# Optimization experiments

Hardware: AMD Instinct MI355X
Metric: run time of the kernel (lower is better)

## Reference

```python
import jax, jax.numpy as jnp
import numpy as np

N_HEADS = 8
D_K = 256
SCALE = D_K ** -0.5


def setup_inputs() -> dict:
    key = jax.random.key(0)
    k1, k2, k3 = jax.random.split(key, 3)
    B, C, H, W = 8, 256, 32, 32
    x = jax.random.normal(k1, (B, C, H, W), dtype=jnp.float32)
    Wp = jax.random.normal(k2, (C, N_HEADS * D_K * 3), dtype=jnp.float32) * (C ** -0.5)
    bp = jnp.zeros((N_HEADS * D_K * 3,), dtype=jnp.float32)
    Wo = jax.random.normal(k3, (N_HEADS * D_K, C), dtype=jnp.float32) * ((N_HEADS * D_K) ** -0.5)
    bo = jnp.zeros((C,), dtype=jnp.float32)
    return {"x": x, "Wp": Wp, "bp": bp, "Wo": Wo, "bo": bo}


def reference(x, Wp, bp, Wo, bo):
    B, C, H, W = x.shape
    S = H * W
    # [B,C,H,W] -> [B,S,C] tokens
    xt = x.reshape(B, C, S).transpose(0, 2, 1)
    qkv = (xt @ Wp + bp).reshape(B, S, N_HEADS, 3 * D_K)
    q, k, v = jnp.split(qkv, 3, axis=-1)  # each [B,S,H,dk]
    attn = jnp.einsum('bihd,bjhd->bijh', q, k) * SCALE
    attn = jax.nn.softmax(attn, axis=2)  # over j (keys)
    res = jnp.einsum('bijh,bjhd->bihd', attn, v).reshape(B, S, N_HEADS * D_K)
    res = res @ Wo + bo + xt  # residual
    return res.transpose(0, 2, 1).reshape(B, C, H, W)
```

## Files before the change

### kernel.cpp

```cpp
#include <hip/hip_runtime.h>

#define NH    8
#define DK    256
#define SS    1024
#define QSCALE 0.09016844136947155f
#define TSH   8192

using frag8  = __attribute__((ext_vector_type(8))) short;
using f32x4  = __attribute__((ext_vector_type(4))) float;
using f32x16 = __attribute__((ext_vector_type(16))) float;

__device__ __forceinline__ unsigned short f2bf(float f) {
    unsigned int u = __float_as_uint(f);
    return (unsigned short)((u + 0x7FFFu + ((u >> 16) & 1u)) >> 16);
}

__device__ __forceinline__ void load_lds16(const void* g, void* l) {
    __builtin_amdgcn_global_load_lds(
        (const __attribute__((address_space(1))) unsigned int*)g,
        (__attribute__((address_space(3))) unsigned int*)l, 16, 0, 0);
}


__global__ __launch_bounds__(256) void k0_t(const float* __restrict__ in,
                                            unsigned short* __restrict__ out,
                                            int R, int C)
{
    __shared__ float tile[32][33];
    const int bz = blockIdx.z;
    const int c0 = blockIdx.x * 32, r0 = blockIdx.y * 32;
    const int tx = threadIdx.x & 31, ty = threadIdx.x >> 5;
    const float* ip = in + (size_t)bz * R * C;
    unsigned short* op = out + (size_t)bz * R * C;
#pragma unroll
    for (int j = 0; j < 4; j++)
        tile[ty + j * 8][tx] = ip[(size_t)(r0 + ty + j * 8) * C + c0 + tx];
    __syncthreads();
#pragma unroll
    for (int j = 0; j < 4; j++)
        op[(size_t)(c0 + ty + j * 8) * R + r0 + tx] = f2bf(tile[tx][ty + j * 8]);
}

__global__ __launch_bounds__(256) void k1_qkv(
    const unsigned short* __restrict__ xb, const unsigned short* __restrict__ Wpt,
    const float* __restrict__ bp,
    unsigned short* __restrict__ qb, unsigned short* __restrict__ kb,
    unsigned short* __restrict__ vb)
{
    __shared__ unsigned short As[128 * 32];
    __shared__ unsigned short Bs[128 * 32];
    const int t = threadIdx.x;
    const int wave = t >> 6, lane = t & 63;
    const int quad = lane >> 4, l16 = lane & 15;
    const int n0 = blockIdx.x * 128, m0 = blockIdx.y * 128;
    const int b = m0 >> 10, s0 = m0 & 1023;
    const int mq = (wave >> 1) * 64, nq = (wave & 1) * 64;
    const int lr = lane >> 2, lc = (lane & 3) * 8;

    const unsigned short* Ag = xb + (size_t)(b * 1024 + s0) * 256;
    const unsigned short* Bg = Wpt + (size_t)n0 * 256;

    f32x4 acc[4][4];
#pragma unroll
    for (int i = 0; i < 4; i++)
#pragma unroll
        for (int j = 0; j < 4; j++) acc[i][j] = (f32x4){0.f, 0.f, 0.f, 0.f};

    for (int k0 = 0; k0 < 256; k0 += 32) {
#pragma unroll
        for (int j = 0; j < 2; j++) {
            int ch = wave + j * 4;
            load_lds16(Ag + (size_t)(ch * 16 + lr) * 256 + k0 + lc, &As[ch * 512]);
            load_lds16(Bg + (size_t)(ch * 16 + lr) * 256 + k0 + lc, &Bs[ch * 512]);
        }
        __syncthreads();
        frag8 af[4], bf[4];
#pragma unroll
        for (int i = 0; i < 4; i++)
            af[i] = *(const frag8*)(&As[(mq + i * 16 + l16) * 32 + quad * 8]);
#pragma unroll
        for (int j = 0; j < 4; j++)
            bf[j] = *(const frag8*)(&Bs[(nq + j * 16 + l16) * 32 + quad * 8]);
#pragma unroll
        for (int i = 0; i < 4; i++)
#pragma unroll
            for (int j = 0; j < 4; j++)
                acc[i][j] = __builtin_amdgcn_mfma_f32_16x16x32_bf16(af[i], bf[j], acc[i][j], 0, 0, 0);
        __syncthreads();
    }

    const int h = n0 / 768;
    const int rem = n0 - h * 768;
    const int tt = rem >> 8;
    const int dbase = (rem & 255) + nq;
    const size_t bh = (size_t)(b * NH + h);
    float bias[4];
#pragma unroll
    for (int j = 0; j < 4; j++) bias[j] = bp[n0 + nq + j * 16 + l16];

    if (tt < 2) {
        const float sc = (tt == 0) ? QSCALE : 1.0f;
        unsigned short* dst = (tt == 0 ? qb : kb) + bh * 32 * TSH;
#pragma unroll
        for (int i = 0; i < 4; i++)
#pragma unroll
            for (int r = 0; r < 4; r++) {
                int s = s0 + mq + i * 16 + quad * 4 + r;
                const size_t tb = (size_t)(s >> 5) * TSH + (s & 31) * 8;
#pragma unroll
                for (int j = 0; j < 4; j++) {
                    int d = dbase + j * 16 + l16;
                    dst[tb + (d >> 3) * 256 + (d & 7)] = f2bf((acc[i][j][r] + bias[j]) * sc);
                }
            }
    } else {
        unsigned short* dst = vb + bh * 32 * TSH;
#pragma unroll
        for (int j = 0; j < 4; j++) {
            int d = dbase + j * 16 + l16;
#pragma unroll
            for (int i = 0; i < 4; i++)
#pragma unroll
                for (int r = 0; r < 4; r++) {
                    int s = s0 + mq + i * 16 + quad * 4 + r;
                    dst[(size_t)(s >> 5) * TSH + ((s >> 3) & 3) * 2048 + d * 8 + (s & 7)]
                        = f2bf(acc[i][j][r] + bias[j]);
                }
        }
    }
}

__global__ __launch_bounds__(256, 2) void k2_attn(
    const unsigned short* __restrict__ qb, const unsigned short* __restrict__ kb,
    const unsigned short* __restrict__ vb, unsigned short* __restrict__ ob)
{
    __shared__ unsigned short Ks[2][TSH];
    __shared__ unsigned short Vs[2][TSH];

    const int t = threadIdx.x;
    const int wave = t >> 6, lane = t & 63;
    const int l32 = lane & 31, hw = lane >> 5;

    const int flat = blockIdx.x;
    const int xcd = flat & 7, tt2 = flat >> 3;
    const int qt = tt2 & 7;
    const int bh = xcd * 8 + (tt2 >> 3);

    const int qrow0 = qt * 128 + wave * 32;

    frag8 qf[16];
    {
        const unsigned short* qp = qb + ((size_t)bh * 32 + qt * 4 + wave) * TSH
                                 + hw * 256 + l32 * 8;
#pragma unroll
        for (int s = 0; s < 16; s++) qf[s] = *(const frag8*)(qp + s * 512);
    }

    f32x16 acc[8];
#pragma unroll
    for (int nb = 0; nb < 8; nb++)
#pragma unroll
        for (int r = 0; r < 16; r++) acc[nb][r] = 0.f;
    float lsum = 0.f;

    const unsigned short* kt0 = kb + (size_t)bh * 32 * TSH;
    const unsigned short* vt0 = vb + (size_t)bh * 32 * TSH;

#pragma unroll
    for (int j = 0; j < 4; j++) {
        int c = wave * 4 + j;
        load_lds16(kt0 + c * 512 + lane * 8, &Ks[0][c * 512]);
        load_lds16(vt0 + c * 512 + lane * 8, &Vs[0][c * 512]);
    }
    __syncthreads();

    for (int kt = 0; kt < 32; kt++) {
        const int cur = kt & 1;

        if (kt < 31) {
            const unsigned short* kg = kt0 + (size_t)(kt + 1) * TSH;
            const unsigned short* vg = vt0 + (size_t)(kt + 1) * TSH;
#pragma unroll
            for (int j = 0; j < 4; j++) {
                int c = wave * 4 + j;
                load_lds16(kg + c * 512 + lane * 8, &Ks[cur ^ 1][c * 512]);
                load_lds16(vg + c * 512 + lane * 8, &Vs[cur ^ 1][c * 512]);
            }
        }

        f32x16 sa0, sa1;
#pragma unroll
        for (int r = 0; r < 16; r++) { sa0[r] = 0.f; sa1[r] = 0.f; }
#pragma unroll
        for (int s = 0; s < 16; s += 2) {
            frag8 kf0 = *(const frag8*)(&Ks[cur][(2 * s + hw) * 256 + l32 * 8]);
            frag8 kf1 = *(const frag8*)(&Ks[cur][(2 * s + 2 + hw) * 256 + l32 * 8]);
            sa0 = __builtin_amdgcn_mfma_f32_32x32x16_bf16(kf0, qf[s], sa0, 0, 0, 0);
            sa1 = __builtin_amdgcn_mfma_f32_32x32x16_bf16(kf1, qf[s + 1], sa1, 0, 0, 0);
        }

        frag8 pf[2];
#pragma unroll
        for (int half = 0; half < 2; half++) {
            float p[8], px[8];
#pragma unroll
            for (int e = 0; e < 8; e++) {
                p[e] = exp2f(sa0[half * 8 + e] + sa1[half * 8 + e]);
                lsum += p[e];
            }
#pragma unroll
            for (int e = 0; e < 8; e++) px[e] = __shfl_xor(p[e], 32);
            frag8 w;
#pragma unroll
            for (int j = 0; j < 4; j++) {
                w[j]     = (short)f2bf(hw ? px[4 + j] : p[j]);
                w[4 + j] = (short)f2bf(hw ? p[4 + j] : px[j]);
            }
            pf[half] = w;
        }

#pragma unroll
        for (int s01 = 0; s01 < 2; s01++)
#pragma unroll
            for (int nb = 0; nb < 8; nb++) {
                frag8 vf = *(const frag8*)(&Vs[cur][(s01 * 2 + hw) * 2048 + (nb * 32 + l32) * 8]);
                acc[nb] = __builtin_amdgcn_mfma_f32_32x32x16_bf16(pf[s01], vf, acc[nb], 0, 0, 0);
            }

        __syncthreads();
    }

    lsum += __shfl_xor(lsum, 32);
    const float linv = 1.f / lsum;

    unsigned short* og = ob + ((size_t)bh * SS + qrow0) * DK + l32;
#pragma unroll
    for (int r = 0; r < 16; r++) {
        const int rowl = (r & 3) + 8 * (r >> 2) + 4 * hw;
        const float li = __shfl(linv, rowl, 64);
        unsigned short* orow = og + (size_t)rowl * DK;
#pragma unroll
        for (int nb = 0; nb < 8; nb++)
            orow[nb * 32] = f2bf(acc[nb][r] * li);
    }
}

__global__ __launch_bounds__(256) void k3_proj(
    const unsigned short* __restrict__ ob, const unsigned short* __restrict__ Wot,
    const float* __restrict__ bo, const float* __restrict__ x,
    float* __restrict__ out)
{
    __shared__ unsigned short As[64 * 32];
    __shared__ unsigned short Bs[64 * 32];
    const int t = threadIdx.x;
    const int wave = t >> 6, lane = t & 63;
    const int quad = lane >> 4, l16 = lane & 15;
    const int n0 = blockIdx.x * 64, m0 = blockIdx.y * 64;
    const int b = m0 >> 10, s0 = m0 & 1023;
    const int mq = (wave >> 1) * 32, nq = (wave & 1) * 32;
    const int lr = lane >> 2, lc = (lane & 3) * 8;

    const unsigned short* Bg = Wot + (size_t)n0 * 2048;

    f32x4 acc[2][2];
#pragma unroll
    for (int i = 0; i < 2; i++)
#pragma unroll
        for (int j = 0; j < 2; j++) acc[i][j] = (f32x4){0.f, 0.f, 0.f, 0.f};

    for (int k0 = 0; k0 < 2048; k0 += 32) {
        const int h = k0 >> 8, d0 = k0 & 255;
        const unsigned short* Ag = ob + (size_t)((b * 8 + h) * 1024 + s0) * 256 + d0;
        load_lds16(Ag + (size_t)(wave * 16 + lr) * 256 + lc, &As[wave * 512]);
        load_lds16(Bg + (size_t)(wave * 16 + lr) * 2048 + k0 + lc, &Bs[wave * 512]);
        __syncthreads();
        frag8 af[2], bf[2];
#pragma unroll
        for (int i = 0; i < 2; i++)
            af[i] = *(const frag8*)(&As[(mq + i * 16 + l16) * 32 + quad * 8]);
#pragma unroll
        for (int j = 0; j < 2; j++)
            bf[j] = *(const frag8*)(&Bs[(nq + j * 16 + l16) * 32 + quad * 8]);
#pragma unroll
        for (int i = 0; i < 2; i++)
#pragma unroll
            for (int j = 0; j < 2; j++)
                acc[i][j] = __builtin_amdgcn_mfma_f32_16x16x32_bf16(af[i], bf[j], acc[i][j], 0, 0, 0);
        __syncthreads();
    }

#pragma unroll
    for (int j = 0; j < 2; j++) {
        int c = n0 + nq + j * 16 + l16;
        float bias = bo[c];
#pragma unroll
        for (int i = 0; i < 2; i++) {
            int s = s0 + mq + i * 16 + quad * 4;
            size_t off = (size_t)(b * 256 + c) * 1024 + s;
            float4 xv = *(const float4*)(&x[off]);
            float4 ov;
            ov.x = acc[i][j][0] + bias + xv.x;
            ov.y = acc[i][j][1] + bias + xv.y;
            ov.z = acc[i][j][2] + bias + xv.z;
            ov.w = acc[i][j][3] + bias + xv.w;
            *(float4*)(&out[off]) = ov;
        }
    }
}

extern "C" void kernel_launch(void* const* d_in, const int* in_sizes, int n_in,
                              void* d_out, int out_size, void* d_ws, size_t ws_size,
                              hipStream_t stream)
{
    const float* x  = (const float*)d_in[0];
    const float* Wp = (const float*)d_in[1];
    const float* bp = (const float*)d_in[2];
    const float* Wo = (const float*)d_in[3];
    const float* bo = (const float*)d_in[4];
    float* out = (float*)d_out;

    char* ws = (char*)d_ws;
    unsigned short* qb  = (unsigned short*)(ws);
    unsigned short* kb  = (unsigned short*)(ws + 33554432);
    unsigned short* vb  = (unsigned short*)(ws + 67108864);
    unsigned short* xb  = (unsigned short*)(ws + 100663296);
    unsigned short* Wpt = (unsigned short*)(ws + 104857600);
    unsigned short* Wot = (unsigned short*)(ws + 108003328);

    k0_t<<<dim3(32, 8, 8), 256, 0, stream>>>(x, xb, 256, 1024);
    k0_t<<<dim3(192, 8, 1), 256, 0, stream>>>(Wp, Wpt, 256, 6144);
    k0_t<<<dim3(8, 64, 1), 256, 0, stream>>>(Wo, Wot, 2048, 256);
    k1_qkv<<<dim3(48, 64), 256, 0, stream>>>(xb, Wpt, bp, qb, kb, vb);
    k2_attn<<<dim3(512), 256, 0, stream>>>(qb, kb, vb, qb );
    k3_proj<<<dim3(4, 128), 256, 0, stream>>>(qb, Wot, bo, x, out);
}
```

Before: 233.9 us.

## Merge transpose launches, vectorize V stores, drop P shuffles, deepen proj K-step

```diff
diff --git a/kernel.cpp b/kernel.cpp
--- a/kernel.cpp
+++ b/kernel.cpp
@@ -14,6 +14,12 @@
     unsigned int u = __float_as_uint(f);
     return (unsigned short)((u + 0x7FFFu + ((u >> 16) & 1u)) >> 16);
 }
+__device__ __forceinline__ unsigned int pk2bf(float lo, float hi) {
+    unsigned int ul = __float_as_uint(lo), uh = __float_as_uint(hi);
+    ul += 0x7FFFu + ((ul >> 16) & 1u);
+    uh += 0x7FFFu + ((uh >> 16) & 1u);
+    return (ul >> 16) | (uh & 0xFFFF0000u);
+}
 
 __device__ __forceinline__ void load_lds16(const void* g, void* l) {
     __builtin_amdgcn_global_load_lds(
@@ -22,23 +28,36 @@
 }
 
 
-__global__ __launch_bounds__(256) void k0_t(const float* __restrict__ in,
-                                            unsigned short* __restrict__ out,
-                                            int R, int C)
+__global__ __launch_bounds__(256) void k0_all(
+    const float* __restrict__ x,  unsigned short* __restrict__ xb,
+    const float* __restrict__ Wp, unsigned short* __restrict__ Wpt,
+    const float* __restrict__ Wo, unsigned short* __restrict__ Wot)
 {
     __shared__ float tile[32][33];
-    const int bz = blockIdx.z;
-    const int c0 = blockIdx.x * 32, r0 = blockIdx.y * 32;
+    const int bid = blockIdx.x;
+    const float* in; unsigned short* out; int R, C, c0, r0;
+    if (bid < 2048) {
+        int rr = bid;
+        in = x + (size_t)(rr >> 8) * 256 * 1024;
+        out = xb + (size_t)(rr >> 8) * 256 * 1024;
+        R = 256; C = 1024; c0 = (rr & 31) * 32; r0 = ((rr >> 5) & 7) * 32;
+    } else if (bid < 3584) {
+        int rr = bid - 2048;
+        in = Wp; out = Wpt; R = 256; C = 6144;
+        c0 = (rr % 192) * 32; r0 = (rr / 192) * 32;
+    } else {
+        int rr = bid - 3584;
+        in = Wo; out = Wot; R = 2048; C = 256;
+        c0 = (rr & 7) * 32; r0 = (rr >> 3) * 32;
+    }
     const int tx = threadIdx.x & 31, ty = threadIdx.x >> 5;
-    const float* ip = in + (size_t)bz * R * C;
-    unsigned short* op = out + (size_t)bz * R * C;
 #pragma unroll
     for (int j = 0; j < 4; j++)
-        tile[ty + j * 8][tx] = ip[(size_t)(r0 + ty + j * 8) * C + c0 + tx];
+        tile[ty + j * 8][tx] = in[(size_t)(r0 + ty + j * 8) * C + c0 + tx];
     __syncthreads();
 #pragma unroll
     for (int j = 0; j < 4; j++)
-        op[(size_t)(c0 + ty + j * 8) * R + r0 + tx] = f2bf(tile[tx][ty + j * 8]);
+        out[(size_t)(c0 + ty + j * 8) * R + r0 + tx] = f2bf(tile[tx][ty + j * 8]);
 }
 
 __global__ __launch_bounds__(256) void k1_qkv(
@@ -115,17 +134,20 @@
             }
     } else {
         unsigned short* dst = vb + bh * 32 * TSH;
+        const int chunk = ((quad & 1)) * 2048;
+        const int jjb = (quad & 2) * 2;
 #pragma unroll
         for (int j = 0; j < 4; j++) {
             int d = dbase + j * 16 + l16;
 #pragma unroll
-            for (int i = 0; i < 4; i++)
-#pragma unroll
-                for (int r = 0; r < 4; r++) {
-                    int s = s0 + mq + i * 16 + quad * 4 + r;
-                    dst[(size_t)(s >> 5) * TSH + ((s >> 3) & 3) * 2048 + d * 8 + (s & 7)]
-                        = f2bf(acc[i][j][r] + bias[j]);
-                }
+            for (int i = 0; i < 4; i++) {
+                int g = ((mq >> 4) + i) & 1;
+                size_t tile = (size_t)((s0 + mq + i * 16) >> 5) * TSH;
+                uint2 st;
+                st.x = pk2bf(acc[i][j][0] + bias[j], acc[i][j][1] + bias[j]);
+                st.y = pk2bf(acc[i][j][2] + bias[j], acc[i][j][3] + bias[j]);
+                *(uint2*)(&dst[tile + g * 4096 + chunk + d * 8 + jjb]) = st;
+            }
         }
     }
 }
@@ -199,32 +221,29 @@
             sa1 = __builtin_amdgcn_mfma_f32_32x32x16_bf16(kf1, qf[s + 1], sa1, 0, 0, 0);
         }
 
+        float p[16];
+#pragma unroll
+        for (int e = 0; e < 16; e++) {
+            p[e] = exp2f(sa0[e] + sa1[e]);
+            lsum += p[e];
+        }
         frag8 pf[2];
 #pragma unroll
-        for (int half = 0; half < 2; half++) {
-            float p[8], px[8];
-#pragma unroll
-            for (int e = 0; e < 8; e++) {
-                p[e] = exp2f(sa0[half * 8 + e] + sa1[half * 8 + e]);
-                lsum += p[e];
-            }
-#pragma unroll
-            for (int e = 0; e < 8; e++) px[e] = __shfl_xor(p[e], 32);
-            frag8 w;
-#pragma unroll
-            for (int j = 0; j < 4; j++) {
-                w[j]     = (short)f2bf(hw ? px[4 + j] : p[j]);
-                w[4 + j] = (short)f2bf(hw ? p[4 + j] : px[j]);
-            }
-            pf[half] = w;
-        }
-
-#pragma unroll
-        for (int s01 = 0; s01 < 2; s01++)
+        for (int g = 0; g < 2; g++) {
+            uint4 w;
+            w.x = pk2bf(p[g * 8 + 0], p[g * 8 + 1]);
+            w.y = pk2bf(p[g * 8 + 2], p[g * 8 + 3]);
+            w.z = pk2bf(p[g * 8 + 4], p[g * 8 + 5]);
+            w.w = pk2bf(p[g * 8 + 6], p[g * 8 + 7]);
+            pf[g] = *(frag8*)&w;
+        }
+
+#pragma unroll
+        for (int g = 0; g < 2; g++)
 #pragma unroll
             for (int nb = 0; nb < 8; nb++) {
-                frag8 vf = *(const frag8*)(&Vs[cur][(s01 * 2 + hw) * 2048 + (nb * 32 + l32) * 8]);
-                acc[nb] = __builtin_amdgcn_mfma_f32_32x32x16_bf16(pf[s01], vf, acc[nb], 0, 0, 0);
+                frag8 vf = *(const frag8*)(&Vs[cur][(g * 2 + hw) * 2048 + (nb * 32 + l32) * 8]);
+                acc[nb] = __builtin_amdgcn_mfma_f32_32x32x16_bf16(pf[g], vf, acc[nb], 0, 0, 0);
             }
 
         __syncthreads();
@@ -250,8 +269,8 @@
     const float* __restrict__ bo, const float* __restrict__ x,
     float* __restrict__ out)
 {
-    __shared__ unsigned short As[64 * 32];
-    __shared__ unsigned short Bs[64 * 32];
+    __shared__ unsigned short As[2][2048];
+    __shared__ unsigned short Bs[2][2048];
     const int t = threadIdx.x;
     const int wave = t >> 6, lane = t & 63;
     const int quad = lane >> 4, l16 = lane & 15;
@@ -268,24 +287,30 @@
 #pragma unroll
         for (int j = 0; j < 2; j++) acc[i][j] = (f32x4){0.f, 0.f, 0.f, 0.f};
 
-    for (int k0 = 0; k0 < 2048; k0 += 32) {
+    for (int k0 = 0; k0 < 2048; k0 += 64) {
         const int h = k0 >> 8, d0 = k0 & 255;
         const unsigned short* Ag = ob + (size_t)((b * 8 + h) * 1024 + s0) * 256 + d0;
-        load_lds16(Ag + (size_t)(wave * 16 + lr) * 256 + lc, &As[wave * 512]);
-        load_lds16(Bg + (size_t)(wave * 16 + lr) * 2048 + k0 + lc, &Bs[wave * 512]);
-        __syncthreads();
-        frag8 af[2], bf[2];
-#pragma unroll
-        for (int i = 0; i < 2; i++)
-            af[i] = *(const frag8*)(&As[(mq + i * 16 + l16) * 32 + quad * 8]);
-#pragma unroll
-        for (int j = 0; j < 2; j++)
-            bf[j] = *(const frag8*)(&Bs[(nq + j * 16 + l16) * 32 + quad * 8]);
-#pragma unroll
-        for (int i = 0; i < 2; i++)
+#pragma unroll
+        for (int sl = 0; sl < 2; sl++) {
+            load_lds16(Ag + (size_t)(wave * 16 + lr) * 256 + sl * 32 + lc, &As[sl][wave * 512]);
+            load_lds16(Bg + (size_t)(wave * 16 + lr) * 2048 + k0 + sl * 32 + lc, &Bs[sl][wave * 512]);
+        }
+        __syncthreads();
+#pragma unroll
+        for (int sl = 0; sl < 2; sl++) {
+            frag8 af[2], bf[2];
+#pragma unroll
+            for (int i = 0; i < 2; i++)
+                af[i] = *(const frag8*)(&As[sl][(mq + i * 16 + l16) * 32 + quad * 8]);
 #pragma unroll
             for (int j = 0; j < 2; j++)
-                acc[i][j] = __builtin_amdgcn_mfma_f32_16x16x32_bf16(af[i], bf[j], acc[i][j], 0, 0, 0);
+                bf[j] = *(const frag8*)(&Bs[sl][(nq + j * 16 + l16) * 32 + quad * 8]);
+#pragma unroll
+            for (int i = 0; i < 2; i++)
+#pragma unroll
+                for (int j = 0; j < 2; j++)
+                    acc[i][j] = __builtin_amdgcn_mfma_f32_16x16x32_bf16(af[i], bf[j], acc[i][j], 0, 0, 0);
+        }
         __syncthreads();
     }
 
@@ -327,9 +352,7 @@
     unsigned short* Wpt = (unsigned short*)(ws + 104857600);
     unsigned short* Wot = (unsigned short*)(ws + 108003328);
 
-    k0_t<<<dim3(32, 8, 8), 256, 0, stream>>>(x, xb, 256, 1024);
-    k0_t<<<dim3(192, 8, 1), 256, 0, stream>>>(Wp, Wpt, 256, 6144);
-    k0_t<<<dim3(8, 64, 1), 256, 0, stream>>>(Wo, Wot, 2048, 256);
+    k0_all<<<dim3(4096), 256, 0, stream>>>(x, xb, Wp, Wpt, Wo, Wot);
     k1_qkv<<<dim3(48, 64), 256, 0, stream>>>(xb, Wpt, bp, qb, kb, vb);
     k2_attn<<<dim3(512), 256, 0, stream>>>(qb, kb, vb, qb );
     k3_proj<<<dim3(4, 128), 256, 0, stream>>>(qb, Wot, bo, x, out);
```

Result: faster. 225.0 us (-3.8%).
